# Performance work log

Hardware: AMD Instinct MI355X
Metric: run time of the kernel (lower is better)

Reference implementation:

```python
import jax, jax.numpy as jnp
import numpy as np

BN_EPS = 1e-5


def setup_inputs() -> dict:
    key = jax.random.key(0)
    ks = jax.random.split(key, 4)
    S, B, F, P, T, H, W = 4, 2, 64, 16, 32, 64, 64
    HID = 32
    feats = jax.random.normal(ks[0], (S, B, F, T, H, W), dtype=jnp.float32)
    p_s = jax.random.normal(ks[1], (B, P, T, H, W), dtype=jnp.float32)
    w1 = jax.random.normal(ks[2], (HID, F + P), dtype=jnp.float32) * (1.0 / np.sqrt(F + P))
    w2 = jax.random.normal(ks[3], (HID,), dtype=jnp.float32) * (1.0 / np.sqrt(HID))
    return {
        "feats": feats,
        "p_s": p_s,
        "w1": w1,
        "bn_gamma": jnp.ones((HID,), jnp.float32),
        "bn_beta": jnp.zeros((HID,), jnp.float32),
        "bn_mean": jnp.zeros((HID,), jnp.float32),
        "bn_var": jnp.ones((HID,), jnp.float32),
        "w2": w2,
        "b2": jnp.zeros((1,), jnp.float32),
    }


def reference(feats, p_s, w1, bn_gamma, bn_beta, bn_mean, bn_var, w2, b2):
    # feats: [S,B,F,T,H,W]; p_s: [B,P,T,H,W]
    F = feats.shape[2]
    w1_f, w1_p = w1[:, :F], w1[:, F:]
    # 1x1x1 conv on concat([f, p_s]) == split contraction; avoids materializing concat
    h = jnp.einsum('of,sbfthw->sbothw', w1_f, feats) \
        + jnp.einsum('op,bpthw->bothw', w1_p, p_s)[None]
    # BatchNorm3d (inference form) folded to scale/shift, then ReLU
    scale = bn_gamma / jnp.sqrt(bn_var + BN_EPS)
    shift = bn_beta - bn_mean * scale
    h = jax.nn.relu(h * scale[:, None, None, None] + shift[:, None, None, None])
    # second 1x1x1 conv: hidden -> 1 logit per branch
    logits = jnp.einsum('sbothw,o->sbthw', h, w2) + b2[0]
    alpha = jax.nn.softmax(logits, axis=0)            # softmax over branches S
    out = jnp.einsum('sbfthw,sbthw->bfthw', feats, alpha)
    return out, jnp.moveaxis(alpha, 0, 1)             # out:[B,F,T,H,W], alpha:[B,S,T,H,W]
```

## Files before the change

### kernel.cpp

```cpp
#include <hip/hip_runtime.h>
#include <hip/hip_bf16.h>
#include <stdint.h>

#define THW   131072
#define NS    4
#define NB    2
#define NF    64
#define NP    16
#define HID   32
#define BN_EPS 1e-5f
#define PXT   128

typedef short  bf16x8  __attribute__((ext_vector_type(8)));
typedef float  f32x16  __attribute__((ext_vector_type(16)));

union FragU { uint32_t u[4]; bf16x8 v; uint4 q; };

__device__ __forceinline__ uint32_t pk2(float a, float b) {
    __hip_bfloat162 h = __float22bfloat162_rn(make_float2(a, b));
    uint32_t r;
    __builtin_memcpy(&r, &h, sizeof(r));
    return r;
}
__device__ __forceinline__ float lo16(uint32_t u) { return __builtin_bit_cast(float, u << 16); }
__device__ __forceinline__ float hi16(uint32_t u) { return __builtin_bit_cast(float, u & 0xFFFF0000u); }

__device__ __forceinline__ void glds16(const float* g, void* l) {
    __builtin_amdgcn_global_load_lds(
        (const __attribute__((address_space(1))) uint32_t*)g,
        (__attribute__((address_space(3))) uint32_t*)l, 16, 0, 0);
}

__global__ __launch_bounds__(256, 2) void gssm_kernel(
    const float* __restrict__ feats, const float* __restrict__ ps,
    const float* __restrict__ w1,    const float* __restrict__ gamma,
    const float* __restrict__ beta,  const float* __restrict__ mean,
    const float* __restrict__ var,   const float* __restrict__ w2,
    float* __restrict__ out)
{
    __shared__ __align__(16) float    fbuf[2][NF][PXT];
    __shared__ __align__(16) float    pbuf[NP][PXT];
    __shared__ __align__(16) uint32_t w1lds[32 * 44];
    __shared__ float2 tbl[HID];

    const int tid  = threadIdx.x;
    const int lane = tid & 63;
    const int wv   = tid >> 6;
    const int hi   = lane >> 5;
    const int ln   = lane & 31;

    for (int t = tid; t < 1280; t += 256) {
        float2 v = ((const float2*)w1)[t];
        int o = t / 40, cp = t - o * 40;
        float sc = gamma[o] * rsqrtf(var[o] + BN_EPS);
        w1lds[o * 44 + (cp >> 3) * 8 + (cp & 7)] = pk2(v.x * sc, v.y * sc);
    }
    if (tid < HID) {
        float sc = gamma[tid] * rsqrtf(var[tid] + BN_EPS);
        tbl[tid] = make_float2(beta[tid] - mean[tid] * sc, w2[tid]);
    }

    const int px0g = blockIdx.x * PXT;
    const int b    = px0g >> 17;
    const int px0  = px0g & (THW - 1);

    const float* featsb = feats + (long)b * NF * THW + px0;
    const float* psb    = ps    + (long)b * NP * THW + px0;
    const long   sstr   = (long)NB * NF * THW;

    const long pl_off = (long)(lane >> 5) * THW + (ln << 2);
    const int  f0     = wv * 16;

    auto stage_feats = [&](int s, int buf) {
        const float* base = featsb + (long)s * sstr;
        #pragma unroll
        for (int i = 0; i < 8; ++i) {
            int f = f0 + i * 2;
            glds16(base + (long)f * THW + pl_off, (void*)&fbuf[buf][f][0]);
        }
    };

    {
        #pragma unroll
        for (int i = 0; i < 2; ++i) {
            int p = wv * 4 + i * 2;
            glds16(psb + (long)p * THW + pl_off, (void*)&pbuf[p][0]);
        }
    }
    stage_feats(0, 0);
    asm volatile("s_waitcnt vmcnt(0) lgkmcnt(0)" ::: "memory");
    __builtin_amdgcn_s_barrier();

    FragU afr[5];
    {
        const uint32_t abase = (uint32_t)(ln * 44 + hi * 4);
        #pragma unroll
        for (int k = 0; k < 5; ++k)
            afr[k].q = *((const uint4*)&w1lds[abase + k * 8]);
    }
    float sh[16], wo[16];
    #pragma unroll
    for (int r = 0; r < 16; ++r) {
        float2 t = tbl[(r & 3) + 8 * (r >> 2) + 4 * hi];
        sh[r] = t.x;
        wo[r] = t.y;
    }

    const int pxloc = wv * 32 + ln;

    FragU bp;
    #pragma unroll
    for (int r = 0; r < 4; ++r)
        bp.u[r] = pk2(pbuf[hi * 8 + 2 * r][pxloc], pbuf[hi * 8 + 2 * r + 1][pxloc]);

    auto consume = [&](int buf, FragU* pk) -> float {
        #pragma unroll
        for (int kb = 0; kb < 4; ++kb)
            #pragma unroll
            for (int r = 0; r < 4; ++r)
                pk[kb].u[r] = pk2(fbuf[buf][kb * 16 + hi * 8 + 2 * r][pxloc],
                                  fbuf[buf][kb * 16 + hi * 8 + 2 * r + 1][pxloc]);
        f32x16 acc;
        #pragma unroll
        for (int r = 0; r < 16; ++r) acc[r] = 0.f;
        acc = __builtin_amdgcn_mfma_f32_32x32x16_bf16(afr[4].v, bp.v,    acc, 0, 0, 0);
        acc = __builtin_amdgcn_mfma_f32_32x32x16_bf16(afr[0].v, pk[0].v, acc, 0, 0, 0);
        acc = __builtin_amdgcn_mfma_f32_32x32x16_bf16(afr[1].v, pk[1].v, acc, 0, 0, 0);
        acc = __builtin_amdgcn_mfma_f32_32x32x16_bf16(afr[2].v, pk[2].v, acc, 0, 0, 0);
        acc = __builtin_amdgcn_mfma_f32_32x32x16_bf16(afr[3].v, pk[3].v, acc, 0, 0, 0);
        float pp[4] = {0.f, 0.f, 0.f, 0.f};
        #pragma unroll
        for (int r = 0; r < 16; ++r) {
            float h = fmaxf(acc[r] + sh[r], 0.f);
            pp[r & 3] = fmaf(h, wo[r], pp[r & 3]);
        }
        float part = (pp[0] + pp[1]) + (pp[2] + pp[3]);
        return part + __shfl_xor(part, 32);
    };

    FragU pk0[4], pk1[4], pk2f[4], pk3[4];
    float lg0, lg1, lg2, lg3;

    stage_feats(1, 1);
    lg0 = consume(0, pk0);
    asm volatile("s_waitcnt vmcnt(0)" ::: "memory");
    __builtin_amdgcn_s_barrier();

    stage_feats(2, 0);
    lg1 = consume(1, pk1);
    asm volatile("s_waitcnt vmcnt(0)" ::: "memory");
    __builtin_amdgcn_s_barrier();

    stage_feats(3, 1);
    lg2 = consume(0, pk2f);
    asm volatile("s_waitcnt vmcnt(0)" ::: "memory");
    __builtin_amdgcn_s_barrier();

    lg3 = consume(1, pk3);

    const float m   = fmaxf(fmaxf(lg0, lg1), fmaxf(lg2, lg3));
    const float e0  = __expf(lg0 - m), e1 = __expf(lg1 - m);
    const float e2  = __expf(lg2 - m), e3 = __expf(lg3 - m);
    const float inv = 1.f / (e0 + e1 + e2 + e3);
    const float a0 = e0 * inv, a1 = e1 * inv, a2 = e2 * inv, a3 = e3 * inv;

    const int thw = px0 + pxloc;

    float* ob = out + ((long)(b * NF + hi * 8)) * THW + thw;
    #pragma unroll
    for (int k = 0; k < 4; ++k)
        #pragma unroll
        for (int r = 0; r < 4; ++r) {
            float vlo = a0 * lo16(pk0[k].u[r]);
            float vhi = a0 * hi16(pk0[k].u[r]);
            vlo = fmaf(a1, lo16(pk1[k].u[r]), vlo);
            vhi = fmaf(a1, hi16(pk1[k].u[r]), vhi);
            vlo = fmaf(a2, lo16(pk2f[k].u[r]), vlo);
            vhi = fmaf(a2, hi16(pk2f[k].u[r]), vhi);
            vlo = fmaf(a3, lo16(pk3[k].u[r]), vlo);
            vhi = fmaf(a3, hi16(pk3[k].u[r]), vhi);
            ob[(long)(k * 16 + 2 * r)     * THW] = vlo;
            ob[(long)(k * 16 + 2 * r + 1) * THW] = vhi;
        }

    float* ab = out + (long)NB * NF * THW + ((long)(b * NS + hi * 2)) * THW + thw;
    ab[0]   = hi ? a2 : a0;
    ab[THW] = hi ? a3 : a1;
}

extern "C" void kernel_launch(void* const* d_in, const int* in_sizes, int n_in,
                              void* d_out, int out_size, void* d_ws, size_t ws_size,
                              hipStream_t stream) {
    const float* feats = (const float*)d_in[0];
    const float* ps    = (const float*)d_in[1];
    const float* w1    = (const float*)d_in[2];
    const float* gamma = (const float*)d_in[3];
    const float* beta  = (const float*)d_in[4];
    const float* mean  = (const float*)d_in[5];
    const float* var   = (const float*)d_in[6];
    const float* w2    = (const float*)d_in[7];
    float* out = (float*)d_out;

    dim3 grid(2048), block(256);
    hipLaunchKernelGGL(gssm_kernel, grid, block, 0, stream,
                       feats, ps, w1, gamma, beta, mean, var, w2, out);
}
```

Measured before the change: 95.96 us.

## Stage feats through registers as packed bf16 LDS with bigger tiles

Replaces direct global-to-LDS fp32 loads with register loads that are packed to bf16 before the LDS write, halving LDS footprint and removing repeated conversion in the consumer. The tile grows to 256 pixels per 512-thread block, and tile order is bit-reversed across blocks to spread memory access. Prefetch of the next branch is held in registers while the current one is consumed, which raises register pressure and may limit occupancy.

```diff
diff --git a/kernel.cpp b/kernel.cpp
--- a/kernel.cpp
+++ b/kernel.cpp
@@ -9,7 +9,7 @@
 #define NP    16
 #define HID   32
 #define BN_EPS 1e-5f
-#define PXT   128
+#define PXT   256
 
 typedef short  bf16x8  __attribute__((ext_vector_type(8)));
 typedef float  f32x16  __attribute__((ext_vector_type(16)));
@@ -25,21 +25,15 @@
 __device__ __forceinline__ float lo16(uint32_t u) { return __builtin_bit_cast(float, u << 16); }
 __device__ __forceinline__ float hi16(uint32_t u) { return __builtin_bit_cast(float, u & 0xFFFF0000u); }
 
-__device__ __forceinline__ void glds16(const float* g, void* l) {
-    __builtin_amdgcn_global_load_lds(
-        (const __attribute__((address_space(1))) uint32_t*)g,
-        (__attribute__((address_space(3))) uint32_t*)l, 16, 0, 0);
-}
-
-__global__ __launch_bounds__(256, 2) void gssm_kernel(
+__global__ __launch_bounds__(512, 2) void gssm_kernel(
     const float* __restrict__ feats, const float* __restrict__ ps,
     const float* __restrict__ w1,    const float* __restrict__ gamma,
     const float* __restrict__ beta,  const float* __restrict__ mean,
     const float* __restrict__ var,   const float* __restrict__ w2,
     float* __restrict__ out)
 {
-    __shared__ __align__(16) float    fbuf[2][NF][PXT];
-    __shared__ __align__(16) float    pbuf[NP][PXT];
+    __shared__ __align__(16) uint32_t fbuf[2][NF / 2][PXT];
+    __shared__ __align__(16) uint32_t pbuf[NP / 2][PXT];
     __shared__ __align__(16) uint32_t w1lds[32 * 44];
     __shared__ float2 tbl[HID];
 
@@ -49,7 +43,7 @@
     const int hi   = lane >> 5;
     const int ln   = lane & 31;
 
-    for (int t = tid; t < 1280; t += 256) {
+    for (int t = tid; t < 1280; t += 512) {
         float2 v = ((const float2*)w1)[t];
         int o = t / 40, cp = t - o * 40;
         float sc = gamma[o] * rsqrtf(var[o] + BN_EPS);
@@ -60,7 +54,8 @@
         tbl[tid] = make_float2(beta[tid] - mean[tid] * sc, w2[tid]);
     }
 
-    const int px0g = blockIdx.x * PXT;
+    const int tile = (int)(__brev((unsigned)blockIdx.x) >> 22);
+    const int px0g = tile * PXT;
     const int b    = px0g >> 17;
     const int px0  = px0g & (THW - 1);
 
@@ -68,28 +63,42 @@
     const float* psb    = ps    + (long)b * NP * THW + px0;
     const long   sstr   = (long)NB * NF * THW;
 
-    const long pl_off = (long)(lane >> 5) * THW + (ln << 2);
-    const int  f0     = wv * 16;
-
-    auto stage_feats = [&](int s, int buf) {
+    auto stage_load = [&](int s, float4* v) {
         const float* base = featsb + (long)s * sstr;
         #pragma unroll
-        for (int i = 0; i < 8; ++i) {
-            int f = f0 + i * 2;
-            glds16(base + (long)f * THW + pl_off, (void*)&fbuf[buf][f][0]);
+        for (int i = 0; i < 4; ++i) {
+            const int fp = wv * 4 + i;
+            v[2 * i]     = ((const float4*)(base + (long)(2 * fp)     * THW))[lane];
+            v[2 * i + 1] = ((const float4*)(base + (long)(2 * fp + 1) * THW))[lane];
         }
     };
-
-    {
-        #pragma unroll
-        for (int i = 0; i < 2; ++i) {
-            int p = wv * 4 + i * 2;
-            glds16(psb + (long)p * THW + pl_off, (void*)&pbuf[p][0]);
-        }
-    }
-    stage_feats(0, 0);
-    asm volatile("s_waitcnt vmcnt(0) lgkmcnt(0)" ::: "memory");
-    __builtin_amdgcn_s_barrier();
+    auto stage_write = [&](const float4* v, int buf) {
+        #pragma unroll
+        for (int i = 0; i < 4; ++i) {
+            const int fp = wv * 4 + i;
+            uint4 w;
+            w.x = pk2(v[2 * i].x, v[2 * i + 1].x);
+            w.y = pk2(v[2 * i].y, v[2 * i + 1].y);
+            w.z = pk2(v[2 * i].z, v[2 * i + 1].z);
+            w.w = pk2(v[2 * i].w, v[2 * i + 1].w);
+            *((uint4*)&fbuf[buf][fp][lane * 4]) = w;
+        }
+    };
+
+    {
+        float4 pa = ((const float4*)(psb + (long)(2 * wv)     * THW))[lane];
+        float4 pb = ((const float4*)(psb + (long)(2 * wv + 1) * THW))[lane];
+        uint4 w;
+        w.x = pk2(pa.x, pb.x);
+        w.y = pk2(pa.y, pb.y);
+        w.z = pk2(pa.z, pb.z);
+        w.w = pk2(pa.w, pb.w);
+        *((uint4*)&pbuf[wv][lane * 4]) = w;
+        float4 v0[8];
+        stage_load(0, v0);
+        stage_write(v0, 0);
+    }
+    __syncthreads();
 
     FragU afr[5];
     {
@@ -111,15 +120,14 @@
     FragU bp;
     #pragma unroll
     for (int r = 0; r < 4; ++r)
-        bp.u[r] = pk2(pbuf[hi * 8 + 2 * r][pxloc], pbuf[hi * 8 + 2 * r + 1][pxloc]);
+        bp.u[r] = pbuf[hi * 4 + r][pxloc];
 
     auto consume = [&](int buf, FragU* pk) -> float {
         #pragma unroll
         for (int kb = 0; kb < 4; ++kb)
             #pragma unroll
             for (int r = 0; r < 4; ++r)
-                pk[kb].u[r] = pk2(fbuf[buf][kb * 16 + hi * 8 + 2 * r][pxloc],
-                                  fbuf[buf][kb * 16 + hi * 8 + 2 * r + 1][pxloc]);
+                pk[kb].u[r] = fbuf[buf][kb * 8 + hi * 4 + r][pxloc];
         f32x16 acc;
         #pragma unroll
         for (int r = 0; r < 16; ++r) acc[r] = 0.f;
@@ -141,20 +149,32 @@
     FragU pk0[4], pk1[4], pk2f[4], pk3[4];
     float lg0, lg1, lg2, lg3;
 
-    stage_feats(1, 1);
-    lg0 = consume(0, pk0);
-    asm volatile("s_waitcnt vmcnt(0)" ::: "memory");
-    __builtin_amdgcn_s_barrier();
-
-    stage_feats(2, 0);
-    lg1 = consume(1, pk1);
-    asm volatile("s_waitcnt vmcnt(0)" ::: "memory");
-    __builtin_amdgcn_s_barrier();
-
-    stage_feats(3, 1);
-    lg2 = consume(0, pk2f);
-    asm volatile("s_waitcnt vmcnt(0)" ::: "memory");
-    __builtin_amdgcn_s_barrier();
+    {
+        float4 v1[8];
+        stage_load(1, v1);
+        asm volatile("" ::: "memory");
+        lg0 = consume(0, pk0);
+        stage_write(v1, 1);
+    }
+    __syncthreads();
+
+    {
+        float4 v2[8];
+        stage_load(2, v2);
+        asm volatile("" ::: "memory");
+        lg1 = consume(1, pk1);
+        stage_write(v2, 0);
+    }
+    __syncthreads();
+
+    {
+        float4 v3[8];
+        stage_load(3, v3);
+        asm volatile("" ::: "memory");
+        lg2 = consume(0, pk2f);
+        stage_write(v3, 1);
+    }
+    __syncthreads();
 
     lg3 = consume(1, pk3);
 
@@ -201,7 +221,7 @@
     const float* w2    = (const float*)d_in[7];
     float* out = (float*)d_out;
 
-    dim3 grid(2048), block(256);
+    dim3 grid(1024), block(512);
     hipLaunchKernelGGL(gssm_kernel, grid, block, 0, stream,
                        feats, ps, w1, gamma, beta, mean, var, w2, out);
 }
```

New measurement: 87.64 us. 1.1x faster.

## Stage feats through registers, pack bf16 into LDS, bit-reverse tile order

Applied to the files above, without the earlier changes.

Replaces the direct global-to-LDS loads with ordinary float2 global loads held in registers. The values are converted to packed bf16 before being written to LDS, which halves LDS footprint and removes the per-consume conversion. A two-deep register prefetch (vA/vB) overlaps the next branch's global loads with MFMA compute, and barriers now wait only on LDS counters. Tile order is bit-reversed across blocks to spread memory traffic, and the BN shift and w2 table is read from LDS inside consume instead of being held in registers. The trade-off is much higher VGPR pressure from the staged registers, and the VMEM waits now fall on the compiler's placement rather than explicit waits.

```diff
diff --git a/kernel.cpp b/kernel.cpp
--- a/kernel.cpp
+++ b/kernel.cpp
@@ -25,10 +25,9 @@
 __device__ __forceinline__ float lo16(uint32_t u) { return __builtin_bit_cast(float, u << 16); }
 __device__ __forceinline__ float hi16(uint32_t u) { return __builtin_bit_cast(float, u & 0xFFFF0000u); }
 
-__device__ __forceinline__ void glds16(const float* g, void* l) {
-    __builtin_amdgcn_global_load_lds(
-        (const __attribute__((address_space(1))) uint32_t*)g,
-        (__attribute__((address_space(3))) uint32_t*)l, 16, 0, 0);
+__device__ __forceinline__ void lds_barrier() {
+    asm volatile("s_waitcnt lgkmcnt(0)" ::: "memory");
+    __builtin_amdgcn_s_barrier();
 }
 
 __global__ __launch_bounds__(256, 2) void gssm_kernel(
@@ -38,8 +37,8 @@
     const float* __restrict__ var,   const float* __restrict__ w2,
     float* __restrict__ out)
 {
-    __shared__ __align__(16) float    fbuf[2][NF][PXT];
-    __shared__ __align__(16) float    pbuf[NP][PXT];
+    __shared__ __align__(16) uint32_t fbuf[2][NF / 2][PXT];
+    __shared__ __align__(16) uint32_t pbuf[NP / 2][PXT];
     __shared__ __align__(16) uint32_t w1lds[32 * 44];
     __shared__ float2 tbl[HID];
 
@@ -60,7 +59,8 @@
         tbl[tid] = make_float2(beta[tid] - mean[tid] * sc, w2[tid]);
     }
 
-    const int px0g = blockIdx.x * PXT;
+    const int tile = (int)(__brev((unsigned)blockIdx.x) >> 21);
+    const int px0g = tile * PXT;
     const int b    = px0g >> 17;
     const int px0  = px0g & (THW - 1);
 
@@ -68,28 +68,43 @@
     const float* psb    = ps    + (long)b * NP * THW + px0;
     const long   sstr   = (long)NB * NF * THW;
 
-    const long pl_off = (long)(lane >> 5) * THW + (ln << 2);
-    const int  f0     = wv * 16;
-
-    auto stage_feats = [&](int s, int buf) {
+    auto stage_load = [&](int s, float2* v) {
         const float* base = featsb + (long)s * sstr;
         #pragma unroll
         for (int i = 0; i < 8; ++i) {
-            int f = f0 + i * 2;
-            glds16(base + (long)f * THW + pl_off, (void*)&fbuf[buf][f][0]);
+            const int fp = wv * 8 + i;
+            v[2 * i]     = ((const float2*)(base + (long)(2 * fp)     * THW))[lane];
+            v[2 * i + 1] = ((const float2*)(base + (long)(2 * fp + 1) * THW))[lane];
         }
     };
-
+    auto stage_write = [&](const float2* v, int buf) {
+        #pragma unroll
+        for (int i = 0; i < 8; ++i) {
+            const int fp = wv * 8 + i;
+            uint2 w;
+            w.x = pk2(v[2 * i].x, v[2 * i + 1].x);
+            w.y = pk2(v[2 * i].y, v[2 * i + 1].y);
+            *((uint2*)&fbuf[buf][fp][2 * lane]) = w;
+        }
+    };
+
+    float2 vA[16], vB[16];
     {
         #pragma unroll
         for (int i = 0; i < 2; ++i) {
-            int p = wv * 4 + i * 2;
-            glds16(psb + (long)p * THW + pl_off, (void*)&pbuf[p][0]);
-        }
-    }
-    stage_feats(0, 0);
-    asm volatile("s_waitcnt vmcnt(0) lgkmcnt(0)" ::: "memory");
-    __builtin_amdgcn_s_barrier();
+            const int pp = wv * 2 + i;
+            float2 a = ((const float2*)(psb + (long)(2 * pp)     * THW))[lane];
+            float2 c = ((const float2*)(psb + (long)(2 * pp + 1) * THW))[lane];
+            uint2 w;
+            w.x = pk2(a.x, c.x);
+            w.y = pk2(a.y, c.y);
+            *((uint2*)&pbuf[pp][2 * lane]) = w;
+        }
+        stage_load(0, vA);
+        stage_write(vA, 0);
+        stage_load(1, vA);
+    }
+    lds_barrier();
 
     FragU afr[5];
     {
@@ -98,28 +113,20 @@
         for (int k = 0; k < 5; ++k)
             afr[k].q = *((const uint4*)&w1lds[abase + k * 8]);
     }
-    float sh[16], wo[16];
-    #pragma unroll
-    for (int r = 0; r < 16; ++r) {
-        float2 t = tbl[(r & 3) + 8 * (r >> 2) + 4 * hi];
-        sh[r] = t.x;
-        wo[r] = t.y;
-    }
 
     const int pxloc = wv * 32 + ln;
 
     FragU bp;
     #pragma unroll
     for (int r = 0; r < 4; ++r)
-        bp.u[r] = pk2(pbuf[hi * 8 + 2 * r][pxloc], pbuf[hi * 8 + 2 * r + 1][pxloc]);
+        bp.u[r] = pbuf[hi * 4 + r][pxloc];
 
     auto consume = [&](int buf, FragU* pk) -> float {
         #pragma unroll
         for (int kb = 0; kb < 4; ++kb)
             #pragma unroll
             for (int r = 0; r < 4; ++r)
-                pk[kb].u[r] = pk2(fbuf[buf][kb * 16 + hi * 8 + 2 * r][pxloc],
-                                  fbuf[buf][kb * 16 + hi * 8 + 2 * r + 1][pxloc]);
+                pk[kb].u[r] = fbuf[buf][kb * 8 + hi * 4 + r][pxloc];
         f32x16 acc;
         #pragma unroll
         for (int r = 0; r < 16; ++r) acc[r] = 0.f;
@@ -128,33 +135,38 @@
         acc = __builtin_amdgcn_mfma_f32_32x32x16_bf16(afr[1].v, pk[1].v, acc, 0, 0, 0);
         acc = __builtin_amdgcn_mfma_f32_32x32x16_bf16(afr[2].v, pk[2].v, acc, 0, 0, 0);
         acc = __builtin_amdgcn_mfma_f32_32x32x16_bf16(afr[3].v, pk[3].v, acc, 0, 0, 0);
-        float pp[4] = {0.f, 0.f, 0.f, 0.f};
+        float pp4[4] = {0.f, 0.f, 0.f, 0.f};
         #pragma unroll
         for (int r = 0; r < 16; ++r) {
-            float h = fmaxf(acc[r] + sh[r], 0.f);
-            pp[r & 3] = fmaf(h, wo[r], pp[r & 3]);
-        }
-        float part = (pp[0] + pp[1]) + (pp[2] + pp[3]);
+            float2 t = tbl[(r & 3) + 8 * (r >> 2) + 4 * hi];
+            float h = fmaxf(acc[r] + t.x, 0.f);
+            pp4[r & 3] = fmaf(h, t.y, pp4[r & 3]);
+        }
+        float part = (pp4[0] + pp4[1]) + (pp4[2] + pp4[3]);
         return part + __shfl_xor(part, 32);
     };
 
     FragU pk0[4], pk1[4], pk2f[4], pk3[4];
     float lg0, lg1, lg2, lg3;
 
-    stage_feats(1, 1);
+    stage_load(2, vB);
+    asm volatile("" ::: "memory");
     lg0 = consume(0, pk0);
-    asm volatile("s_waitcnt vmcnt(0)" ::: "memory");
-    __builtin_amdgcn_s_barrier();
-
-    stage_feats(2, 0);
+    asm volatile("" ::: "memory");
+    stage_write(vA, 1);
+    lds_barrier();
+
+    stage_load(3, vA);
+    asm volatile("" ::: "memory");
     lg1 = consume(1, pk1);
-    asm volatile("s_waitcnt vmcnt(0)" ::: "memory");
-    __builtin_amdgcn_s_barrier();
-
-    stage_feats(3, 1);
+    asm volatile("" ::: "memory");
+    stage_write(vB, 0);
+    lds_barrier();
+
     lg2 = consume(0, pk2f);
-    asm volatile("s_waitcnt vmcnt(0)" ::: "memory");
-    __builtin_amdgcn_s_barrier();
+    asm volatile("" ::: "memory");
+    stage_write(vA, 1);
+    lds_barrier();
 
     lg3 = consume(1, pk3);
 
```

After: 88.41 us. -7.9%, faster.

## Issue all four branch loads upfront with smaller tiles and bit-reversed tile order

Applied to the files above, without the earlier changes.

Shrinks each block to 64 pixels and 128 threads, doubling the grid. All four branch feature tiles now load into LDS at once, and staged vmcnt waits let each branch be consumed as soon as it arrives, replacing the old double-buffered reload after each barrier. Tile index is bit-reversed from blockIdx to spread concurrent blocks across memory. This puts more loads in flight per block, at the cost of more LDS per block (64KB+ fbuf) and possibly lower occupancy.

```diff
diff --git a/kernel.cpp b/kernel.cpp
--- a/kernel.cpp
+++ b/kernel.cpp
@@ -9,7 +9,7 @@
 #define NP    16
 #define HID   32
 #define BN_EPS 1e-5f
-#define PXT   128
+#define PXT   64
 
 typedef short  bf16x8  __attribute__((ext_vector_type(8)));
 typedef float  f32x16  __attribute__((ext_vector_type(16)));
@@ -31,14 +31,14 @@
         (__attribute__((address_space(3))) uint32_t*)l, 16, 0, 0);
 }
 
-__global__ __launch_bounds__(256, 2) void gssm_kernel(
+__global__ __launch_bounds__(128, 2) void gssm_kernel(
     const float* __restrict__ feats, const float* __restrict__ ps,
     const float* __restrict__ w1,    const float* __restrict__ gamma,
     const float* __restrict__ beta,  const float* __restrict__ mean,
     const float* __restrict__ var,   const float* __restrict__ w2,
     float* __restrict__ out)
 {
-    __shared__ __align__(16) float    fbuf[2][NF][PXT];
+    __shared__ __align__(16) float    fbuf[NS][NF][PXT];
     __shared__ __align__(16) float    pbuf[NP][PXT];
     __shared__ __align__(16) uint32_t w1lds[32 * 44];
     __shared__ float2 tbl[HID];
@@ -49,7 +49,7 @@
     const int hi   = lane >> 5;
     const int ln   = lane & 31;
 
-    for (int t = tid; t < 1280; t += 256) {
+    for (int t = tid; t < 1280; t += 128) {
         float2 v = ((const float2*)w1)[t];
         int o = t / 40, cp = t - o * 40;
         float sc = gamma[o] * rsqrtf(var[o] + BN_EPS);
@@ -59,8 +59,10 @@
         float sc = gamma[tid] * rsqrtf(var[tid] + BN_EPS);
         tbl[tid] = make_float2(beta[tid] - mean[tid] * sc, w2[tid]);
     }
-
-    const int px0g = blockIdx.x * PXT;
+    asm volatile("s_waitcnt vmcnt(0)" ::: "memory");
+
+    const int tile = (int)(__brev((unsigned)blockIdx.x) >> 20);
+    const int px0g = tile * PXT;
     const int b    = px0g >> 17;
     const int px0  = px0g & (THW - 1);
 
@@ -68,27 +70,24 @@
     const float* psb    = ps    + (long)b * NP * THW + px0;
     const long   sstr   = (long)NB * NF * THW;
 
-    const long pl_off = (long)(lane >> 5) * THW + (ln << 2);
-    const int  f0     = wv * 16;
-
-    auto stage_feats = [&](int s, int buf) {
+    const long lsub = (long)(lane >> 4) * THW + (long)(lane & 15) * 4;
+
+    #pragma unroll
+    for (int j = 0; j < 2; ++j) {
+        const int p4 = wv * 8 + j * 4;
+        glds16(psb + (long)p4 * THW + lsub, (void*)&pbuf[p4][0]);
+    }
+    #pragma unroll
+    for (int s = 0; s < NS; ++s) {
         const float* base = featsb + (long)s * sstr;
         #pragma unroll
         for (int i = 0; i < 8; ++i) {
-            int f = f0 + i * 2;
-            glds16(base + (long)f * THW + pl_off, (void*)&fbuf[buf][f][0]);
+            const int f4 = wv * 32 + i * 4;
+            glds16(base + (long)f4 * THW + lsub, (void*)&fbuf[s][f4][0]);
         }
-    };
-
-    {
-        #pragma unroll
-        for (int i = 0; i < 2; ++i) {
-            int p = wv * 4 + i * 2;
-            glds16(psb + (long)p * THW + pl_off, (void*)&pbuf[p][0]);
-        }
-    }
-    stage_feats(0, 0);
-    asm volatile("s_waitcnt vmcnt(0) lgkmcnt(0)" ::: "memory");
+    }
+
+    asm volatile("s_waitcnt lgkmcnt(0)" ::: "memory");
     __builtin_amdgcn_s_barrier();
 
     FragU afr[5];
@@ -109,17 +108,14 @@
     const int pxloc = wv * 32 + ln;
 
     FragU bp;
-    #pragma unroll
-    for (int r = 0; r < 4; ++r)
-        bp.u[r] = pk2(pbuf[hi * 8 + 2 * r][pxloc], pbuf[hi * 8 + 2 * r + 1][pxloc]);
-
-    auto consume = [&](int buf, FragU* pk) -> float {
+
+    auto consume = [&](int s, FragU* pk) -> float {
         #pragma unroll
         for (int kb = 0; kb < 4; ++kb)
             #pragma unroll
             for (int r = 0; r < 4; ++r)
-                pk[kb].u[r] = pk2(fbuf[buf][kb * 16 + hi * 8 + 2 * r][pxloc],
-                                  fbuf[buf][kb * 16 + hi * 8 + 2 * r + 1][pxloc]);
+                pk[kb].u[r] = pk2(fbuf[s][kb * 16 + hi * 8 + 2 * r][pxloc],
+                                  fbuf[s][kb * 16 + hi * 8 + 2 * r + 1][pxloc]);
         f32x16 acc;
         #pragma unroll
         for (int r = 0; r < 16; ++r) acc[r] = 0.f;
@@ -128,35 +124,37 @@
         acc = __builtin_amdgcn_mfma_f32_32x32x16_bf16(afr[1].v, pk[1].v, acc, 0, 0, 0);
         acc = __builtin_amdgcn_mfma_f32_32x32x16_bf16(afr[2].v, pk[2].v, acc, 0, 0, 0);
         acc = __builtin_amdgcn_mfma_f32_32x32x16_bf16(afr[3].v, pk[3].v, acc, 0, 0, 0);
-        float pp[4] = {0.f, 0.f, 0.f, 0.f};
+        float pp4[4] = {0.f, 0.f, 0.f, 0.f};
         #pragma unroll
         for (int r = 0; r < 16; ++r) {
             float h = fmaxf(acc[r] + sh[r], 0.f);
-            pp[r & 3] = fmaf(h, wo[r], pp[r & 3]);
+            pp4[r & 3] = fmaf(h, wo[r], pp4[r & 3]);
         }
-        float part = (pp[0] + pp[1]) + (pp[2] + pp[3]);
+        float part = (pp4[0] + pp4[1]) + (pp4[2] + pp4[3]);
         return part + __shfl_xor(part, 32);
     };
 
     FragU pk0[4], pk1[4], pk2f[4], pk3[4];
     float lg0, lg1, lg2, lg3;
 
-    stage_feats(1, 1);
+    asm volatile("s_waitcnt vmcnt(24)" ::: "memory");
+    __builtin_amdgcn_s_barrier();
+    #pragma unroll
+    for (int r = 0; r < 4; ++r)
+        bp.u[r] = pk2(pbuf[hi * 8 + 2 * r][pxloc], pbuf[hi * 8 + 2 * r + 1][pxloc]);
     lg0 = consume(0, pk0);
+
+    asm volatile("s_waitcnt vmcnt(16)" ::: "memory");
+    __builtin_amdgcn_s_barrier();
+    lg1 = consume(1, pk1);
+
+    asm volatile("s_waitcnt vmcnt(8)" ::: "memory");
+    __builtin_amdgcn_s_barrier();
+    lg2 = consume(2, pk2f);
+
     asm volatile("s_waitcnt vmcnt(0)" ::: "memory");
     __builtin_amdgcn_s_barrier();
-
-    stage_feats(2, 0);
-    lg1 = consume(1, pk1);
-    asm volatile("s_waitcnt vmcnt(0)" ::: "memory");
-    __builtin_amdgcn_s_barrier();
-
-    stage_feats(3, 1);
-    lg2 = consume(0, pk2f);
-    asm volatile("s_waitcnt vmcnt(0)" ::: "memory");
-    __builtin_amdgcn_s_barrier();
-
-    lg3 = consume(1, pk3);
+    lg3 = consume(3, pk3);
 
     const float m   = fmaxf(fmaxf(lg0, lg1), fmaxf(lg2, lg3));
     const float e0  = __expf(lg0 - m), e1 = __expf(lg1 - m);
@@ -201,7 +199,7 @@
     const float* w2    = (const float*)d_in[7];
     float* out = (float*)d_out;
 
-    dim3 grid(2048), block(256);
+    dim3 grid(4096), block(128);
     hipLaunchKernelGGL(gssm_kernel, grid, block, 0, stream,
                        feats, ps, w1, gamma, beta, mean, var, w2, out);
 }
```

New measurement: 97.53 us. Within noise of the previous version (+1.6%).
